# Kernel optimization log

Hardware: AMD Instinct MI355X
Metric: run time of the kernel (lower is better)

Reference implementation:

```python
import jax, jax.numpy as jnp
import numpy as np

N_EDGES = 4096
HIDDEN = 256
EDGE_DIM = 128
NUM_HEADS = 4
NUM_GRAPHS = 64


def setup_inputs() -> dict:
    key0 = jax.random.key(0)
    ks = jax.random.split(key0, 10)
    s = 0.02
    inp = {
        "query": jax.random.normal(ks[0], (N_EDGES, HIDDEN), jnp.float32),
        "key": jax.random.normal(ks[1], (N_EDGES, EDGE_DIM), jnp.float32),
        "value": jax.random.normal(ks[2], (N_EDGES, EDGE_DIM), jnp.float32),
        "edge_graph_index": jnp.sort(
            jax.random.randint(ks[3], (N_EDGES,), 0, NUM_GRAPHS)
        ),
        # edge_proj: Linear(edge_context_dim -> hidden_dim)
        "w_edge": jax.random.normal(ks[4], (HIDDEN, EDGE_DIM), jnp.float32) * s,
        "b_edge": jnp.zeros((HIDDEN,), jnp.float32),
        # nn.MultiheadAttention packed in-projection [3H, H] and bias [3H]
        "w_in": jax.random.normal(ks[5], (3 * HIDDEN, HIDDEN), jnp.float32) * s,
        "b_in": jnp.zeros((3 * HIDDEN,), jnp.float32),
        # out_proj: Linear(hidden -> hidden)
        "w_out": jax.random.normal(ks[6], (HIDDEN, HIDDEN), jnp.float32) * s,
        "b_out": jnp.zeros((HIDDEN,), jnp.float32),
    }
    return inp


def reference(query, key, value, edge_graph_index,
              w_edge, b_edge, w_in, b_in, w_out, b_out):
    # Segment-wise cross attention == block-diagonal masked attention over all edges.
    N, H = query.shape
    nh = NUM_HEADS
    dh = H // nh

    # edge feature projection (applied to both key and value, as in the module)
    K = key @ w_edge.T + b_edge      # [N, H]
    V = value @ w_edge.T + b_edge    # [N, H]

    wq, wk, wv = jnp.split(w_in, 3, axis=0)
    bq, bk, bv = jnp.split(b_in, 3)
    Qh = (query @ wq.T + bq).reshape(N, nh, dh)
    Kh = (K @ wk.T + bk).reshape(N, nh, dh)
    Vh = (V @ wv.T + bv).reshape(N, nh, dh)

    scale = 1.0 / jnp.sqrt(jnp.asarray(dh, query.dtype))
    scores = jnp.einsum("nhd,mhd->hnm", Qh, Kh) * scale  # [nh, N, N]

    # attention only within the same graph segment
    same_graph = edge_graph_index[:, None] == edge_graph_index[None, :]  # [N, N]
    neg = jnp.finfo(scores.dtype).min
    scores = jnp.where(same_graph[None, :, :], scores, neg)

    attn = jax.nn.softmax(scores, axis=-1)                 # [nh, N, N]
    out = jnp.einsum("hnm,mhd->nhd", attn, Vh).reshape(N, H)
    out = out @ w_out.T + b_out
    return query + out
```

## Files before the change

kernel.cpp:

```cpp
#include <hip/hip_runtime.h>

#define N_EDGES 4096
#define HIDDEN  256
#define EDGE_DIM 128
#define NUM_HEADS 4
#define NUM_GRAPHS 64
#define DH 64

typedef __attribute__((ext_vector_type(8))) short short8;
typedef __attribute__((ext_vector_type(4))) float f32x4;

__device__ __forceinline__ unsigned short f2bf(float f) {
  unsigned u = __builtin_bit_cast(unsigned, f);
  u += 0x7FFF + ((u >> 16) & 1);
  return (unsigned short)(u >> 16);
}
__device__ __forceinline__ float bf2f(unsigned short u) {
  return __builtin_bit_cast(float, (unsigned)u << 16);
}
__device__ __forceinline__ short8 cvt8(float4 x, float4 y) {
  short8 v;
  v[0] = (short)f2bf(x.x); v[1] = (short)f2bf(x.y);
  v[2] = (short)f2bf(x.z); v[3] = (short)f2bf(x.w);
  v[4] = (short)f2bf(y.x); v[5] = (short)f2bf(y.y);
  v[6] = (short)f2bf(y.z); v[7] = (short)f2bf(y.w);
  return v;
}
__device__ __forceinline__ float4 us4f(ushort4 v) {
  float4 f;
  f.x = bf2f(v.x); f.y = bf2f(v.y); f.z = bf2f(v.z); f.w = bf2f(v.w);
  return f;
}

__device__ __forceinline__ int lbound(const int* __restrict__ a, int n, int v) {
  int lo = 0, hi = n;
  while (lo < hi) { int mid = (lo + hi) >> 1; if (a[mid] < v) lo = mid + 1; else hi = mid; }
  return lo;
}

template<bool ABF, bool OUTF32>
__device__ __forceinline__ void gemm_core(const void* Ap, const float* W,
                                          const float* bias, const float* res,
                                          void* Cp, const int K) {
  const int t = threadIdx.x;
  const int m0 = blockIdx.x * 64, n0 = blockIdx.y * 64;
  __shared__ unsigned short As[64 * 40];
  __shared__ unsigned short Ws[64 * 40];
  const int r = t >> 2, kg = t & 3;
  const int lane = t & 63, w = t >> 6;
  const int quad = lane >> 4, l16 = lane & 15;
  const int wm = (w >> 1) * 32, wn = (w & 1) * 32;
  f32x4 acc[2][2] = {};
  const float* pw = W + (size_t)(n0 + r) * K + kg * 8;
  float4 w0 = *(const float4*)(pw), w1 = *(const float4*)(pw + 4);
  const unsigned short* pa16 = (const unsigned short*)Ap + (size_t)(m0 + r) * K + kg * 8;
  const float* pa32 = (const float*)Ap + (size_t)(m0 + r) * K + kg * 8;
  short8 a16; float4 a0, a1;
  if (ABF) a16 = *(const short8*)pa16;
  else { a0 = *(const float4*)pa32; a1 = *(const float4*)(pa32 + 4); }
  for (int kc = 0; kc < K; kc += 32) {
    short8 na16; float4 na0, na1, nw0, nw1;
    if (kc + 32 < K) {
      if (ABF) na16 = *(const short8*)(pa16 + kc + 32);
      else { na0 = *(const float4*)(pa32 + kc + 32); na1 = *(const float4*)(pa32 + kc + 36); }
      nw0 = *(const float4*)(pw + kc + 32); nw1 = *(const float4*)(pw + kc + 36);
    }
    __syncthreads();
    short8 av = ABF ? a16 : cvt8(a0, a1);
    *(short8*)&As[r * 40 + kg * 8] = av;
    *(short8*)&Ws[r * 40 + kg * 8] = cvt8(w0, w1);
    __syncthreads();
    short8 af0 = *(const short8*)&As[(wm + l16) * 40 + quad * 8];
    short8 af1 = *(const short8*)&As[(wm + 16 + l16) * 40 + quad * 8];
    short8 bf0 = *(const short8*)&Ws[(wn + l16) * 40 + quad * 8];
    short8 bf1 = *(const short8*)&Ws[(wn + 16 + l16) * 40 + quad * 8];
    acc[0][0] = __builtin_amdgcn_mfma_f32_16x16x32_bf16(af0, bf0, acc[0][0], 0, 0, 0);
    acc[0][1] = __builtin_amdgcn_mfma_f32_16x16x32_bf16(af0, bf1, acc[0][1], 0, 0, 0);
    acc[1][0] = __builtin_amdgcn_mfma_f32_16x16x32_bf16(af1, bf0, acc[1][0], 0, 0, 0);
    acc[1][1] = __builtin_amdgcn_mfma_f32_16x16x32_bf16(af1, bf1, acc[1][1], 0, 0, 0);
    a16 = na16; a0 = na0; a1 = na1; w0 = nw0; w1 = nw1;
  }
#pragma unroll
  for (int j = 0; j < 2; ++j) {
    const int col = n0 + wn + j * 16 + l16;
    const float bj = bias[col];
#pragma unroll
    for (int i = 0; i < 2; ++i) {
#pragma unroll
      for (int reg = 0; reg < 4; ++reg) {
        const int row = m0 + wm + i * 16 + quad * 4 + reg;
        const size_t idx = (size_t)row * HIDDEN + col;
        float v = acc[i][j][reg] + bj;
        if (OUTF32) ((float*)Cp)[idx] = v + res[idx];
        else        ((unsigned short*)Cp)[idx] = f2bf(v);
      }
    }
  }
}

__global__ __launch_bounds__(256) void proj1(const float* __restrict__ query,
                                             const float* __restrict__ key,
                                             const float* __restrict__ value,
                                             const float* __restrict__ w_in,
                                             const float* __restrict__ b_in,
                                             const float* __restrict__ w_edge,
                                             const float* __restrict__ b_edge,
                                             const int* __restrict__ gidx,
                                             unsigned short* Qh, unsigned short* Ek,
                                             unsigned short* Ev, int* segStart) {
  if (blockIdx.z == 0 && blockIdx.x == 0 && blockIdx.y == 0 && threadIdx.x <= NUM_GRAPHS)
    segStart[threadIdx.x] = lbound(gidx, N_EDGES, threadIdx.x);
  if (blockIdx.z == 0)      gemm_core<false, false>(query, w_in,   b_in,   nullptr, Qh, 256);
  else if (blockIdx.z == 1) gemm_core<false, false>(key,   w_edge, b_edge, nullptr, Ek, 128);
  else                      gemm_core<false, false>(value, w_edge, b_edge, nullptr, Ev, 128);
}

__global__ __launch_bounds__(256) void proj2(const unsigned short* __restrict__ Ek,
                                             const unsigned short* __restrict__ Ev,
                                             const float* __restrict__ w_in,
                                             const float* __restrict__ b_in,
                                             unsigned short* Kh, unsigned short* Vh) {
  if (blockIdx.z == 0) gemm_core<true, false>(Ek, w_in + 256 * HIDDEN, b_in + 256, nullptr, Kh, 256);
  else                 gemm_core<true, false>(Ev, w_in + 512 * HIDDEN, b_in + 512, nullptr, Vh, 256);
}

__global__ __launch_bounds__(256) void attn_segment(const unsigned short* __restrict__ Qh,
                                                    const unsigned short* __restrict__ Kh,
                                                    const unsigned short* __restrict__ Vh,
                                                    const int* __restrict__ segStart,
                                                    unsigned short* __restrict__ ao) {
  const int graph = blockIdx.x, h = blockIdx.y, zg = blockIdx.z;
  const int segLo = segStart[graph];
  const int segHi = segStart[graph + 1];
  const int segLen = segHi - segLo;
  const int t = threadIdx.x, lane = t & 63, w = t >> 6;
  __shared__ float Qs[16][68], Ks[64][68], Vs[64][68];
  __shared__ float Ps[4][64][4];
  const float scale = 0.125f;
  const int r0 = w * 4;

  for (int chunk = zg; chunk * 16 < segLen; chunk += 8) {
    const int row0 = segLo + chunk * 16;
    const int rows = min(16, segHi - row0);
    __syncthreads();
    { int r = t >> 4, d4 = (t & 15) * 4;
      if (r < rows)
        *(float4*)&Qs[r][d4] =
            us4f(*(const ushort4*)(Qh + (size_t)(row0 + r) * HIDDEN + h * DH + d4)); }

    float accv[4] = {0.f, 0.f, 0.f, 0.f}, lsum[4] = {0.f, 0.f, 0.f, 0.f};

    for (int c0 = segLo; c0 < segHi; c0 += 64) {
      const int tc = min(64, segHi - c0);
      __syncthreads();
#pragma unroll
      for (int it = 0; it < 4; ++it) {
        int s = t + it * 256; int j = s >> 4; int d4 = (s & 15) * 4;
        if (j < tc) {
          *(float4*)&Ks[j][d4] =
              us4f(*(const ushort4*)(Kh + (size_t)(c0 + j) * HIDDEN + h * DH + d4));
          *(float4*)&Vs[j][d4] =
              us4f(*(const ushort4*)(Vh + (size_t)(c0 + j) * HIDDEN + h * DH + d4));
        }
      }
      __syncthreads();
      float4 kreg[16];
#pragma unroll
      for (int d4 = 0; d4 < 16; ++d4) kreg[d4] = *(const float4*)&Ks[lane][d4 * 4];
      float p[4];
#pragma unroll
      for (int r = 0; r < 4; ++r) {
        float s = 0.f;
#pragma unroll
        for (int d4 = 0; d4 < 16; ++d4) {
          float4 q = *(const float4*)&Qs[r0 + r][d4 * 4];
          s += q.x * kreg[d4].x + q.y * kreg[d4].y + q.z * kreg[d4].z + q.w * kreg[d4].w;
        }
        p[r] = (lane < tc && r0 + r < rows) ? __expf(s * scale) : 0.f;
        lsum[r] += p[r];
      }
      float4 p4; p4.x = p[0]; p4.y = p[1]; p4.z = p[2]; p4.w = p[3];
      *(float4*)&Ps[w][lane][0] = p4;
      __asm__ volatile("s_waitcnt lgkmcnt(0)" ::: "memory");
      for (int j = 0; j < tc; ++j) {
        const float v = Vs[j][lane];
        float4 pj = *(const float4*)&Ps[w][j][0];
        accv[0] += pj.x * v; accv[1] += pj.y * v;
        accv[2] += pj.z * v; accv[3] += pj.w * v;
      }
    }
#pragma unroll
    for (int off = 32; off; off >>= 1)
#pragma unroll
      for (int r = 0; r < 4; ++r) lsum[r] += __shfl_xor(lsum[r], off);
#pragma unroll
    for (int r = 0; r < 4; ++r)
      if (r0 + r < rows)
        ao[(size_t)(row0 + r0 + r) * HIDDEN + h * DH + lane] = f2bf(accv[r] / lsum[r]);
  }
}

__global__ __launch_bounds__(256) void outproj(const unsigned short* __restrict__ ao,
                                               const float* __restrict__ w_out,
                                               const float* __restrict__ b_out,
                                               const float* __restrict__ query,
                                               float* __restrict__ out) {
  gemm_core<true, true>(ao, w_out, b_out, query, out, 256);
}

extern "C" void kernel_launch(void* const* d_in, const int* in_sizes, int n_in,
                              void* d_out, int out_size, void* d_ws, size_t ws_size,
                              hipStream_t stream) {
  const float* query  = (const float*)d_in[0];
  const float* key    = (const float*)d_in[1];
  const float* value  = (const float*)d_in[2];
  const int*   gidx   = (const int*)d_in[3];
  const float* w_edge = (const float*)d_in[4];
  const float* b_edge = (const float*)d_in[5];
  const float* w_in   = (const float*)d_in[6];
  const float* b_in   = (const float*)d_in[7];
  const float* w_out  = (const float*)d_in[8];
  const float* b_out  = (const float*)d_in[9];
  float* out = (float*)d_out;

  int* segStart = (int*)d_ws;
  unsigned short* Qh = (unsigned short*)((char*)d_ws + 512);
  unsigned short* Ek = Qh + (size_t)N_EDGES * HIDDEN;
  unsigned short* Ev = Ek + (size_t)N_EDGES * HIDDEN;
  unsigned short* Kh = Ev + (size_t)N_EDGES * HIDDEN;
  unsigned short* Vh = Kh + (size_t)N_EDGES * HIDDEN;
  unsigned short* ao = Vh + (size_t)N_EDGES * HIDDEN;

  proj1<<<dim3(64, 4, 3), 256, 0, stream>>>(query, key, value, w_in, b_in,
                                            w_edge, b_edge, gidx, Qh, Ek, Ev, segStart);
  proj2<<<dim3(64, 4, 2), 256, 0, stream>>>(Ek, Ev, w_in, b_in, Kh, Vh);
  attn_segment<<<dim3(NUM_GRAPHS, NUM_HEADS, 8), 256, 0, stream>>>(Qh, Kh, Vh, segStart, ao);
  outproj<<<dim3(64, 4), 256, 0, stream>>>(ao, w_out, b_out, query, out);
}
```

Baseline: 117.9 us.

## Fold edge projection into K/V in-projection weights and retile output projection

Precomputes combined weights Wk = wk·w_edge and Wv = wv·w_edge, plus the folded biases, in a small fp32 kernel. K and V can then be projected straight from the 128-dim inputs in one GEMM instead of two chained GEMMs, which removes the intermediate Ek/Ev buffers and one kernel launch. The output projection also gets its own kernel with 32-row tiles, doubling the grid size to improve occupancy. The weight folding adds a tiny GEMM on every call and changes the bf16 rounding points relative to the reference.

```diff
diff --git a/kernel.cpp b/kernel.cpp
--- a/kernel.cpp
+++ b/kernel.cpp
@@ -38,10 +38,63 @@
   return lo;
 }
 
-template<bool ABF, bool OUTF32>
-__device__ __forceinline__ void gemm_core(const void* Ap, const float* W,
-                                          const float* bias, const float* res,
-                                          void* Cp, const int K) {
+__global__ __launch_bounds__(256) void combine(const float* __restrict__ w_in,
+                                               const float* __restrict__ b_in,
+                                               const float* __restrict__ w_edge,
+                                               const float* __restrict__ b_edge,
+                                               const int* __restrict__ gidx,
+                                               float* __restrict__ Wk, float* __restrict__ Wv,
+                                               float* __restrict__ bkv, int* __restrict__ segStart) {
+  const int kv = blockIdx.z;
+  const float* A = w_in + (size_t)(HIDDEN + kv * HIDDEN) * HIDDEN;
+  float* C = kv ? Wv : Wk;
+  const int m0 = blockIdx.x * 64, n0 = blockIdx.y * 64;
+  const int t = threadIdx.x;
+  if (blockIdx.x == 0 && blockIdx.y == 0 && kv == 0 && t <= NUM_GRAPHS)
+    segStart[t] = lbound(gidx, N_EDGES, t);
+  __shared__ float As[16][68], Bs[16][68];
+  const int arow = t >> 2, ak4 = (t & 3) * 4;
+  const int bkr = t >> 4, bj4 = (t & 15) * 4;
+  const int tx = t & 15, ty = t >> 4;
+  float acc[4][4] = {};
+  for (int kc = 0; kc < HIDDEN; kc += 16) {
+    float4 av = *(const float4*)(A + (size_t)(m0 + arow) * HIDDEN + kc + ak4);
+    float4 bv = *(const float4*)(w_edge + (size_t)(kc + bkr) * EDGE_DIM + n0 + bj4);
+    __syncthreads();
+    As[ak4 + 0][arow] = av.x; As[ak4 + 1][arow] = av.y;
+    As[ak4 + 2][arow] = av.z; As[ak4 + 3][arow] = av.w;
+    *(float4*)&Bs[bkr][bj4] = bv;
+    __syncthreads();
+#pragma unroll
+    for (int kk = 0; kk < 16; ++kk) {
+      float4 a = *(const float4*)&As[kk][ty * 4];
+      float4 b = *(const float4*)&Bs[kk][tx * 4];
+      float ar[4] = {a.x, a.y, a.z, a.w}, br[4] = {b.x, b.y, b.z, b.w};
+#pragma unroll
+      for (int r = 0; r < 4; ++r)
+#pragma unroll
+        for (int c = 0; c < 4; ++c) acc[r][c] += ar[r] * br[c];
+    }
+  }
+#pragma unroll
+  for (int r = 0; r < 4; ++r) {
+    float4 o; o.x = acc[r][0]; o.y = acc[r][1]; o.z = acc[r][2]; o.w = acc[r][3];
+    *(float4*)&C[(size_t)(m0 + ty * 4 + r) * EDGE_DIM + n0 + tx * 4] = o;
+  }
+  if (blockIdx.y == 0) {
+    const int row = m0 + (t >> 2), part = t & 3;
+    float s = 0.f;
+    const float* ar = A + (size_t)row * HIDDEN + part * 64;
+#pragma unroll 8
+    for (int m = 0; m < 64; ++m) s += ar[m] * b_edge[part * 64 + m];
+    s += __shfl_xor(s, 1); s += __shfl_xor(s, 2);
+    if (part == 0) bkv[kv * HIDDEN + row] = s + b_in[HIDDEN + kv * HIDDEN + row];
+  }
+}
+
+__device__ __forceinline__ void gemm_core(const float* Ap, const float* W,
+                                          const float* bias, unsigned short* C,
+                                          const int K) {
   const int t = threadIdx.x;
   const int m0 = blockIdx.x * 64, n0 = blockIdx.y * 64;
   __shared__ unsigned short As[64 * 40];
@@ -52,22 +105,17 @@
   const int wm = (w >> 1) * 32, wn = (w & 1) * 32;
   f32x4 acc[2][2] = {};
   const float* pw = W + (size_t)(n0 + r) * K + kg * 8;
+  const float* pa = Ap + (size_t)(m0 + r) * K + kg * 8;
   float4 w0 = *(const float4*)(pw), w1 = *(const float4*)(pw + 4);
-  const unsigned short* pa16 = (const unsigned short*)Ap + (size_t)(m0 + r) * K + kg * 8;
-  const float* pa32 = (const float*)Ap + (size_t)(m0 + r) * K + kg * 8;
-  short8 a16; float4 a0, a1;
-  if (ABF) a16 = *(const short8*)pa16;
-  else { a0 = *(const float4*)pa32; a1 = *(const float4*)(pa32 + 4); }
+  float4 a0 = *(const float4*)(pa), a1 = *(const float4*)(pa + 4);
   for (int kc = 0; kc < K; kc += 32) {
-    short8 na16; float4 na0, na1, nw0, nw1;
+    float4 na0, na1, nw0, nw1;
     if (kc + 32 < K) {
-      if (ABF) na16 = *(const short8*)(pa16 + kc + 32);
-      else { na0 = *(const float4*)(pa32 + kc + 32); na1 = *(const float4*)(pa32 + kc + 36); }
+      na0 = *(const float4*)(pa + kc + 32); na1 = *(const float4*)(pa + kc + 36);
       nw0 = *(const float4*)(pw + kc + 32); nw1 = *(const float4*)(pw + kc + 36);
     }
     __syncthreads();
-    short8 av = ABF ? a16 : cvt8(a0, a1);
-    *(short8*)&As[r * 40 + kg * 8] = av;
+    *(short8*)&As[r * 40 + kg * 8] = cvt8(a0, a1);
     *(short8*)&Ws[r * 40 + kg * 8] = cvt8(w0, w1);
     __syncthreads();
     short8 af0 = *(const short8*)&As[(wm + l16) * 40 + quad * 8];
@@ -78,7 +126,7 @@
     acc[0][1] = __builtin_amdgcn_mfma_f32_16x16x32_bf16(af0, bf1, acc[0][1], 0, 0, 0);
     acc[1][0] = __builtin_amdgcn_mfma_f32_16x16x32_bf16(af1, bf0, acc[1][0], 0, 0, 0);
     acc[1][1] = __builtin_amdgcn_mfma_f32_16x16x32_bf16(af1, bf1, acc[1][1], 0, 0, 0);
-    a16 = na16; a0 = na0; a1 = na1; w0 = nw0; w1 = nw1;
+    a0 = na0; a1 = na1; w0 = nw0; w1 = nw1;
   }
 #pragma unroll
   for (int j = 0; j < 2; ++j) {
@@ -89,39 +137,25 @@
 #pragma unroll
       for (int reg = 0; reg < 4; ++reg) {
         const int row = m0 + wm + i * 16 + quad * 4 + reg;
-        const size_t idx = (size_t)row * HIDDEN + col;
-        float v = acc[i][j][reg] + bj;
-        if (OUTF32) ((float*)Cp)[idx] = v + res[idx];
-        else        ((unsigned short*)Cp)[idx] = f2bf(v);
+        C[(size_t)row * HIDDEN + col] = f2bf(acc[i][j][reg] + bj);
       }
     }
   }
 }
 
-__global__ __launch_bounds__(256) void proj1(const float* __restrict__ query,
-                                             const float* __restrict__ key,
-                                             const float* __restrict__ value,
-                                             const float* __restrict__ w_in,
-                                             const float* __restrict__ b_in,
-                                             const float* __restrict__ w_edge,
-                                             const float* __restrict__ b_edge,
-                                             const int* __restrict__ gidx,
-                                             unsigned short* Qh, unsigned short* Ek,
-                                             unsigned short* Ev, int* segStart) {
-  if (blockIdx.z == 0 && blockIdx.x == 0 && blockIdx.y == 0 && threadIdx.x <= NUM_GRAPHS)
-    segStart[threadIdx.x] = lbound(gidx, N_EDGES, threadIdx.x);
-  if (blockIdx.z == 0)      gemm_core<false, false>(query, w_in,   b_in,   nullptr, Qh, 256);
-  else if (blockIdx.z == 1) gemm_core<false, false>(key,   w_edge, b_edge, nullptr, Ek, 128);
-  else                      gemm_core<false, false>(value, w_edge, b_edge, nullptr, Ev, 128);
-}
-
-__global__ __launch_bounds__(256) void proj2(const unsigned short* __restrict__ Ek,
-                                             const unsigned short* __restrict__ Ev,
-                                             const float* __restrict__ w_in,
-                                             const float* __restrict__ b_in,
-                                             unsigned short* Kh, unsigned short* Vh) {
-  if (blockIdx.z == 0) gemm_core<true, false>(Ek, w_in + 256 * HIDDEN, b_in + 256, nullptr, Kh, 256);
-  else                 gemm_core<true, false>(Ev, w_in + 512 * HIDDEN, b_in + 512, nullptr, Vh, 256);
+__global__ __launch_bounds__(256) void proj(const float* __restrict__ query,
+                                            const float* __restrict__ key,
+                                            const float* __restrict__ value,
+                                            const float* __restrict__ w_in,
+                                            const float* __restrict__ b_in,
+                                            const float* __restrict__ Wk,
+                                            const float* __restrict__ Wv,
+                                            const float* __restrict__ bkv,
+                                            unsigned short* Qh, unsigned short* Kh,
+                                            unsigned short* Vh) {
+  if (blockIdx.z == 0)      gemm_core(query, w_in, b_in,        Qh, 256);
+  else if (blockIdx.z == 1) gemm_core(key,   Wk,   bkv,         Kh, 128);
+  else                      gemm_core(value, Wv,   bkv + HIDDEN, Vh, 128);
 }
 
 __global__ __launch_bounds__(256) void attn_segment(const unsigned short* __restrict__ Qh,
@@ -205,7 +239,48 @@
                                                const float* __restrict__ b_out,
                                                const float* __restrict__ query,
                                                float* __restrict__ out) {
-  gemm_core<true, true>(ao, w_out, b_out, query, out, 256);
+  const int t = threadIdx.x;
+  const int m0 = blockIdx.x * 32, n0 = blockIdx.y * 64;
+  __shared__ unsigned short As[32 * 40];
+  __shared__ unsigned short Ws[64 * 40];
+  const int lane = t & 63, w = t >> 6;
+  const int quad = lane >> 4, l16 = lane & 15;
+  const int wn = w * 16;
+  const int wr = t >> 2, wkg = t & 3;
+  const int ar = (t & 127) >> 2, akg = t & 3;
+  f32x4 acc[2] = {};
+  const float* pw = w_out + (size_t)(n0 + wr) * HIDDEN + wkg * 8;
+  const unsigned short* pa = ao + (size_t)(m0 + ar) * HIDDEN + akg * 8;
+  short8 a16 = (t < 128) ? *(const short8*)pa : short8{};
+  float4 w0 = *(const float4*)pw, w1 = *(const float4*)(pw + 4);
+  for (int kc = 0; kc < HIDDEN; kc += 32) {
+    short8 na16; float4 nw0, nw1;
+    if (kc + 32 < HIDDEN) {
+      if (t < 128) na16 = *(const short8*)(pa + kc + 32);
+      nw0 = *(const float4*)(pw + kc + 32); nw1 = *(const float4*)(pw + kc + 36);
+    }
+    __syncthreads();
+    if (t < 128) *(short8*)&As[ar * 40 + akg * 8] = a16;
+    *(short8*)&Ws[wr * 40 + wkg * 8] = cvt8(w0, w1);
+    __syncthreads();
+    short8 af0 = *(const short8*)&As[l16 * 40 + quad * 8];
+    short8 af1 = *(const short8*)&As[(16 + l16) * 40 + quad * 8];
+    short8 bf = *(const short8*)&Ws[(wn + l16) * 40 + quad * 8];
+    acc[0] = __builtin_amdgcn_mfma_f32_16x16x32_bf16(af0, bf, acc[0], 0, 0, 0);
+    acc[1] = __builtin_amdgcn_mfma_f32_16x16x32_bf16(af1, bf, acc[1], 0, 0, 0);
+    a16 = na16; w0 = nw0; w1 = nw1;
+  }
+  const int col = n0 + wn + l16;
+  const float bj = b_out[col];
+#pragma unroll
+  for (int i = 0; i < 2; ++i) {
+#pragma unroll
+    for (int reg = 0; reg < 4; ++reg) {
+      const int row = m0 + i * 16 + quad * 4 + reg;
+      const size_t idx = (size_t)row * HIDDEN + col;
+      out[idx] = acc[i][reg] + bj + query[idx];
+    }
+  }
 }
 
 extern "C" void kernel_launch(void* const* d_in, const int* in_sizes, int n_in,
@@ -224,16 +299,18 @@
   float* out = (float*)d_out;
 
   int* segStart = (int*)d_ws;
-  unsigned short* Qh = (unsigned short*)((char*)d_ws + 512);
-  unsigned short* Ek = Qh + (size_t)N_EDGES * HIDDEN;
-  unsigned short* Ev = Ek + (size_t)N_EDGES * HIDDEN;
-  unsigned short* Kh = Ev + (size_t)N_EDGES * HIDDEN;
+  float* Wk  = (float*)((char*)d_ws + 512);
+  float* Wv  = Wk + 32768;
+  float* bkv = Wv + 32768;
+  unsigned short* Qh = (unsigned short*)(bkv + 512);
+  unsigned short* Kh = Qh + (size_t)N_EDGES * HIDDEN;
   unsigned short* Vh = Kh + (size_t)N_EDGES * HIDDEN;
   unsigned short* ao = Vh + (size_t)N_EDGES * HIDDEN;
 
-  proj1<<<dim3(64, 4, 3), 256, 0, stream>>>(query, key, value, w_in, b_in,
-                                            w_edge, b_edge, gidx, Qh, Ek, Ev, segStart);
-  proj2<<<dim3(64, 4, 2), 256, 0, stream>>>(Ek, Ev, w_in, b_in, Kh, Vh);
+  combine<<<dim3(4, 2, 2), 256, 0, stream>>>(w_in, b_in, w_edge, b_edge, gidx,
+                                             Wk, Wv, bkv, segStart);
+  proj<<<dim3(64, 4, 3), 256, 0, stream>>>(query, key, value, w_in, b_in,
+                                           Wk, Wv, bkv, Qh, Kh, Vh);
   attn_segment<<<dim3(NUM_GRAPHS, NUM_HEADS, 8), 256, 0, stream>>>(Qh, Kh, Vh, segStart, ao);
-  outproj<<<dim3(64, 4), 256, 0, stream>>>(ao, w_out, b_out, query, out);
-}
+  outproj<<<dim3(128, 4), 256, 0, stream>>>(ao, w_out, b_out, query, out);
+}
```

New measurement: 132.5 us. 12.4% more time.

## Fuse all stages into one persistent kernel with global atomic barriers

Applied to the files above, without the earlier changes.

Replaces the four separate launches (two projection stages, segment attention, output projection) with a single 512-block persistent kernel whose phases are separated by a software grid barrier built on an atomic counter. The goal is to remove launch overhead and inter-kernel gaps. Attention is now split over 2 z-chunks per graph/head instead of 8, and the output projection uses 32x64 tiles so that 512 blocks cover it. The barrier depends on every block being co-resident and has a spin timeout that could silently break ordering. Attention gets less parallelism than before.

```diff
diff --git a/kernel.cpp b/kernel.cpp
--- a/kernel.cpp
+++ b/kernel.cpp
@@ -38,14 +38,34 @@
   return lo;
 }
 
-template<bool ABF, bool OUTF32>
-__device__ __forceinline__ void gemm_core(const void* Ap, const float* W,
-                                          const float* bias, const float* res,
-                                          void* Cp, const int K) {
+__device__ __forceinline__ void gbar(unsigned* c, unsigned target) {
+  __syncthreads();
+  if (threadIdx.x == 0) {
+    __threadfence();
+    atomicAdd(c, 1u);
+    unsigned spins = 0;
+    while (atomicAdd(c, 0u) < target) {
+      __builtin_amdgcn_s_sleep(2);
+      if (++spins > (1u << 20)) break;
+    }
+    __threadfence();
+  }
+  __syncthreads();
+}
+
+union SharedU {
+  struct { unsigned short As[64 * 40]; unsigned short Ws[64 * 40]; } g;
+  struct { float Qs[16][68]; float Ks[64][68]; float Vs[64][68]; float Ps[4][64][4]; } a;
+};
+
+template<bool ABF>
+__device__ __forceinline__ void gemm_tile(SharedU& sh, int m0, int n0,
+                                          const void* Ap, const float* W,
+                                          const float* bias, unsigned short* C,
+                                          const int K) {
   const int t = threadIdx.x;
-  const int m0 = blockIdx.x * 64, n0 = blockIdx.y * 64;
-  __shared__ unsigned short As[64 * 40];
-  __shared__ unsigned short Ws[64 * 40];
+  unsigned short* As = sh.g.As;
+  unsigned short* Ws = sh.g.Ws;
   const int r = t >> 2, kg = t & 3;
   const int lane = t & 63, w = t >> 6;
   const int quad = lane >> 4, l16 = lane & 15;
@@ -66,8 +86,7 @@
       nw0 = *(const float4*)(pw + kc + 32); nw1 = *(const float4*)(pw + kc + 36);
     }
     __syncthreads();
-    short8 av = ABF ? a16 : cvt8(a0, a1);
-    *(short8*)&As[r * 40 + kg * 8] = av;
+    *(short8*)&As[r * 40 + kg * 8] = ABF ? a16 : cvt8(a0, a1);
     *(short8*)&Ws[r * 40 + kg * 8] = cvt8(w0, w1);
     __syncthreads();
     short8 af0 = *(const short8*)&As[(wm + l16) * 40 + quad * 8];
@@ -89,63 +108,32 @@
 #pragma unroll
       for (int reg = 0; reg < 4; ++reg) {
         const int row = m0 + wm + i * 16 + quad * 4 + reg;
-        const size_t idx = (size_t)row * HIDDEN + col;
-        float v = acc[i][j][reg] + bj;
-        if (OUTF32) ((float*)Cp)[idx] = v + res[idx];
-        else        ((unsigned short*)Cp)[idx] = f2bf(v);
+        C[(size_t)row * HIDDEN + col] = f2bf(acc[i][j][reg] + bj);
       }
     }
   }
 }
 
-__global__ __launch_bounds__(256) void proj1(const float* __restrict__ query,
-                                             const float* __restrict__ key,
-                                             const float* __restrict__ value,
-                                             const float* __restrict__ w_in,
-                                             const float* __restrict__ b_in,
-                                             const float* __restrict__ w_edge,
-                                             const float* __restrict__ b_edge,
-                                             const int* __restrict__ gidx,
-                                             unsigned short* Qh, unsigned short* Ek,
-                                             unsigned short* Ev, int* segStart) {
-  if (blockIdx.z == 0 && blockIdx.x == 0 && blockIdx.y == 0 && threadIdx.x <= NUM_GRAPHS)
-    segStart[threadIdx.x] = lbound(gidx, N_EDGES, threadIdx.x);
-  if (blockIdx.z == 0)      gemm_core<false, false>(query, w_in,   b_in,   nullptr, Qh, 256);
-  else if (blockIdx.z == 1) gemm_core<false, false>(key,   w_edge, b_edge, nullptr, Ek, 128);
-  else                      gemm_core<false, false>(value, w_edge, b_edge, nullptr, Ev, 128);
-}
-
-__global__ __launch_bounds__(256) void proj2(const unsigned short* __restrict__ Ek,
-                                             const unsigned short* __restrict__ Ev,
-                                             const float* __restrict__ w_in,
-                                             const float* __restrict__ b_in,
-                                             unsigned short* Kh, unsigned short* Vh) {
-  if (blockIdx.z == 0) gemm_core<true, false>(Ek, w_in + 256 * HIDDEN, b_in + 256, nullptr, Kh, 256);
-  else                 gemm_core<true, false>(Ev, w_in + 512 * HIDDEN, b_in + 512, nullptr, Vh, 256);
-}
-
-__global__ __launch_bounds__(256) void attn_segment(const unsigned short* __restrict__ Qh,
-                                                    const unsigned short* __restrict__ Kh,
-                                                    const unsigned short* __restrict__ Vh,
-                                                    const int* __restrict__ segStart,
-                                                    unsigned short* __restrict__ ao) {
-  const int graph = blockIdx.x, h = blockIdx.y, zg = blockIdx.z;
+__device__ __forceinline__ void attn_job(SharedU& sh, int graph, int h, int zg, int zstride,
+                                         const unsigned short* __restrict__ Qh,
+                                         const unsigned short* __restrict__ Kh,
+                                         const unsigned short* __restrict__ Vh,
+                                         const int* __restrict__ segStart,
+                                         unsigned short* __restrict__ ao) {
   const int segLo = segStart[graph];
   const int segHi = segStart[graph + 1];
   const int segLen = segHi - segLo;
   const int t = threadIdx.x, lane = t & 63, w = t >> 6;
-  __shared__ float Qs[16][68], Ks[64][68], Vs[64][68];
-  __shared__ float Ps[4][64][4];
   const float scale = 0.125f;
   const int r0 = w * 4;
 
-  for (int chunk = zg; chunk * 16 < segLen; chunk += 8) {
+  for (int chunk = zg; chunk * 16 < segLen; chunk += zstride) {
     const int row0 = segLo + chunk * 16;
     const int rows = min(16, segHi - row0);
     __syncthreads();
     { int r = t >> 4, d4 = (t & 15) * 4;
       if (r < rows)
-        *(float4*)&Qs[r][d4] =
+        *(float4*)&sh.a.Qs[r][d4] =
             us4f(*(const ushort4*)(Qh + (size_t)(row0 + r) * HIDDEN + h * DH + d4)); }
 
     float accv[4] = {0.f, 0.f, 0.f, 0.f}, lsum[4] = {0.f, 0.f, 0.f, 0.f};
@@ -157,34 +145,34 @@
       for (int it = 0; it < 4; ++it) {
         int s = t + it * 256; int j = s >> 4; int d4 = (s & 15) * 4;
         if (j < tc) {
-          *(float4*)&Ks[j][d4] =
+          *(float4*)&sh.a.Ks[j][d4] =
               us4f(*(const ushort4*)(Kh + (size_t)(c0 + j) * HIDDEN + h * DH + d4));
-          *(float4*)&Vs[j][d4] =
+          *(float4*)&sh.a.Vs[j][d4] =
               us4f(*(const ushort4*)(Vh + (size_t)(c0 + j) * HIDDEN + h * DH + d4));
         }
       }
       __syncthreads();
       float4 kreg[16];
 #pragma unroll
-      for (int d4 = 0; d4 < 16; ++d4) kreg[d4] = *(const float4*)&Ks[lane][d4 * 4];
+      for (int d4 = 0; d4 < 16; ++d4) kreg[d4] = *(const float4*)&sh.a.Ks[lane][d4 * 4];
       float p[4];
 #pragma unroll
       for (int r = 0; r < 4; ++r) {
         float s = 0.f;
 #pragma unroll
         for (int d4 = 0; d4 < 16; ++d4) {
-          float4 q = *(const float4*)&Qs[r0 + r][d4 * 4];
+          float4 q = *(const float4*)&sh.a.Qs[r0 + r][d4 * 4];
           s += q.x * kreg[d4].x + q.y * kreg[d4].y + q.z * kreg[d4].z + q.w * kreg[d4].w;
         }
         p[r] = (lane < tc && r0 + r < rows) ? __expf(s * scale) : 0.f;
         lsum[r] += p[r];
       }
       float4 p4; p4.x = p[0]; p4.y = p[1]; p4.z = p[2]; p4.w = p[3];
-      *(float4*)&Ps[w][lane][0] = p4;
+      *(float4*)&sh.a.Ps[w][lane][0] = p4;
       __asm__ volatile("s_waitcnt lgkmcnt(0)" ::: "memory");
       for (int j = 0; j < tc; ++j) {
-        const float v = Vs[j][lane];
-        float4 pj = *(const float4*)&Ps[w][j][0];
+        const float v = sh.a.Vs[j][lane];
+        float4 pj = *(const float4*)&sh.a.Ps[w][j][0];
         accv[0] += pj.x * v; accv[1] += pj.y * v;
         accv[2] += pj.z * v; accv[3] += pj.w * v;
       }
@@ -200,12 +188,100 @@
   }
 }
 
-__global__ __launch_bounds__(256) void outproj(const unsigned short* __restrict__ ao,
+__device__ __forceinline__ void outproj_tile(SharedU& sh, int m0, int n0,
+                                             const unsigned short* __restrict__ ao,
+                                             const float* __restrict__ w_out,
+                                             const float* __restrict__ b_out,
+                                             const float* __restrict__ query,
+                                             float* __restrict__ out) {
+  const int t = threadIdx.x;
+  unsigned short* As = sh.g.As;
+  unsigned short* Ws = sh.g.Ws;
+  const int lane = t & 63, w = t >> 6;
+  const int quad = lane >> 4, l16 = lane & 15;
+  const int wn = w * 16;
+  const int wr = t >> 2, wkg = t & 3;
+  const int ar = (t & 127) >> 2, akg = t & 3;
+  f32x4 acc[2] = {};
+  const float* pw = w_out + (size_t)(n0 + wr) * HIDDEN + wkg * 8;
+  const unsigned short* pa = ao + (size_t)(m0 + ar) * HIDDEN + akg * 8;
+  short8 a16 = (t < 128) ? *(const short8*)pa : short8{};
+  float4 w0 = *(const float4*)pw, w1 = *(const float4*)(pw + 4);
+  for (int kc = 0; kc < HIDDEN; kc += 32) {
+    short8 na16; float4 nw0, nw1;
+    if (kc + 32 < HIDDEN) {
+      if (t < 128) na16 = *(const short8*)(pa + kc + 32);
+      nw0 = *(const float4*)(pw + kc + 32); nw1 = *(const float4*)(pw + kc + 36);
+    }
+    __syncthreads();
+    if (t < 128) *(short8*)&As[ar * 40 + akg * 8] = a16;
+    *(short8*)&Ws[wr * 40 + wkg * 8] = cvt8(w0, w1);
+    __syncthreads();
+    short8 af0 = *(const short8*)&As[l16 * 40 + quad * 8];
+    short8 af1 = *(const short8*)&As[(16 + l16) * 40 + quad * 8];
+    short8 bf = *(const short8*)&Ws[(wn + l16) * 40 + quad * 8];
+    acc[0] = __builtin_amdgcn_mfma_f32_16x16x32_bf16(af0, bf, acc[0], 0, 0, 0);
+    acc[1] = __builtin_amdgcn_mfma_f32_16x16x32_bf16(af1, bf, acc[1], 0, 0, 0);
+    a16 = na16; w0 = nw0; w1 = nw1;
+  }
+  const int col = n0 + wn + l16;
+  const float bj = b_out[col];
+#pragma unroll
+  for (int i = 0; i < 2; ++i) {
+#pragma unroll
+    for (int reg = 0; reg < 4; ++reg) {
+      const int row = m0 + i * 16 + quad * 4 + reg;
+      const size_t idx = (size_t)row * HIDDEN + col;
+      out[idx] = acc[i][reg] + bj + query[idx];
+    }
+  }
+}
+
+__global__ void zero_ctr(unsigned* c) { *c = 0u; }
+
+__global__ __launch_bounds__(256, 2) void mega(const float* __restrict__ query,
+                                               const float* __restrict__ key,
+                                               const float* __restrict__ value,
+                                               const int* __restrict__ gidx,
+                                               const float* __restrict__ w_edge,
+                                               const float* __restrict__ b_edge,
+                                               const float* __restrict__ w_in,
+                                               const float* __restrict__ b_in,
                                                const float* __restrict__ w_out,
                                                const float* __restrict__ b_out,
-                                               const float* __restrict__ query,
-                                               float* __restrict__ out) {
-  gemm_core<true, true>(ao, w_out, b_out, query, out, 256);
+                                               float* __restrict__ out,
+                                               int* __restrict__ segStart,
+                                               unsigned* __restrict__ barrier_ctr,
+                                               unsigned short* Qh, unsigned short* Ek,
+                                               unsigned short* Ev, unsigned short* Kh,
+                                               unsigned short* Vh, unsigned short* ao) {
+  __shared__ SharedU sh;
+  const int b = blockIdx.x;
+
+  if (b == 0 && threadIdx.x <= NUM_GRAPHS)
+    segStart[threadIdx.x] = lbound(gidx, N_EDGES, threadIdx.x);
+  for (int j = b; j < 768; j += 512) {
+    const int z = j >> 8, tile = j & 255;
+    const int m0 = (tile & 63) * 64, n0 = (tile >> 6) * 64;
+    if (z == 0)      gemm_tile<false>(sh, m0, n0, query, w_in,   b_in,   Qh, 256);
+    else if (z == 1) gemm_tile<false>(sh, m0, n0, key,   w_edge, b_edge, Ek, 128);
+    else             gemm_tile<false>(sh, m0, n0, value, w_edge, b_edge, Ev, 128);
+    __syncthreads();
+  }
+  gbar(barrier_ctr, 512);
+
+  {
+    const int z = b >> 8, tile = b & 255;
+    const int m0 = (tile & 63) * 64, n0 = (tile >> 6) * 64;
+    if (z == 0) gemm_tile<true>(sh, m0, n0, Ek, w_in + 256 * HIDDEN, b_in + 256, Kh, 256);
+    else        gemm_tile<true>(sh, m0, n0, Ev, w_in + 512 * HIDDEN, b_in + 512, Vh, 256);
+  }
+  gbar(barrier_ctr, 1024);
+
+  attn_job(sh, b >> 3, (b >> 1) & 3, b & 1, 2, Qh, Kh, Vh, segStart, ao);
+  gbar(barrier_ctr, 1536);
+
+  outproj_tile(sh, (b & 127) * 32, (b >> 7) * 64, ao, w_out, b_out, query, out);
 }
 
 extern "C" void kernel_launch(void* const* d_in, const int* in_sizes, int n_in,
@@ -224,6 +300,7 @@
   float* out = (float*)d_out;
 
   int* segStart = (int*)d_ws;
+  unsigned* barrier_ctr = (unsigned*)d_ws + 96;
   unsigned short* Qh = (unsigned short*)((char*)d_ws + 512);
   unsigned short* Ek = Qh + (size_t)N_EDGES * HIDDEN;
   unsigned short* Ev = Ek + (size_t)N_EDGES * HIDDEN;
@@ -231,9 +308,8 @@
   unsigned short* Vh = Kh + (size_t)N_EDGES * HIDDEN;
   unsigned short* ao = Vh + (size_t)N_EDGES * HIDDEN;
 
-  proj1<<<dim3(64, 4, 3), 256, 0, stream>>>(query, key, value, w_in, b_in,
-                                            w_edge, b_edge, gidx, Qh, Ek, Ev, segStart);
-  proj2<<<dim3(64, 4, 2), 256, 0, stream>>>(Ek, Ev, w_in, b_in, Kh, Vh);
-  attn_segment<<<dim3(NUM_GRAPHS, NUM_HEADS, 8), 256, 0, stream>>>(Qh, Kh, Vh, segStart, ao);
-  outproj<<<dim3(64, 4), 256, 0, stream>>>(ao, w_out, b_out, query, out);
-}
+  zero_ctr<<<1, 1, 0, stream>>>(barrier_ctr);
+  mega<<<512, 256, 0, stream>>>(query, key, value, gidx, w_edge, b_edge,
+                                w_in, b_in, w_out, b_out, out, segStart,
+                                barrier_ctr, Qh, Ek, Ev, Kh, Vh, ao);
+}
```

Result: slower. 273.2 us (+131.7%).
